# Kernel tuning notes

Measured on AMD Instinct MI355X. Metric: run time of the kernel, lower is better.

Reference implementation:

```python
import jax, jax.numpy as jnp
import numpy as np

B, S, D = 2, 1024, 2048      # batch, seq, hidden
E, F, TOP_K = 8, 1408, 2     # experts, moe intermediate, top-k


def setup_inputs() -> dict:
    key = jax.random.key(0)
    k1, k2, k3, k4, k5 = jax.random.split(key, 5)
    scale = 0.02
    return {
        "hidden_states": jax.random.normal(k1, (B, S, D), jnp.float32),
        "gate_w": jax.random.normal(k2, (E, D), jnp.float32) * scale,   # nn.Linear weight [E, D]
        "w_gate": jax.random.normal(k3, (E, D, F), jnp.float32) * scale,  # gate_proj per expert
        "w_up": jax.random.normal(k4, (E, D, F), jnp.float32) * scale,    # up_proj per expert
        "w_down": jax.random.normal(k5, (E, F, D), jnp.float32) * scale,  # down_proj per expert
    }


def reference(hidden_states, gate_w, w_gate, w_up, w_down):
    b, s, d = hidden_states.shape
    e = gate_w.shape[0]
    x = hidden_states.reshape(-1, d)                      # [T, D], T = b*s
    t = x.shape[0]

    # router: logits -> full softmax -> top-k -> renormalize (qwen_topk_softmax, normalize_topk=True)
    logits = x @ gate_w.T                                  # [T, E]
    probs = jax.nn.softmax(logits.astype(jnp.float32), axis=-1)
    top_w, sel = jax.lax.top_k(probs, TOP_K)               # [T, K]
    top_w = top_w / jnp.sum(top_w, axis=-1, keepdims=True)
    top_w = top_w.astype(logits.dtype)

    # per-token per-expert combine weight (0 for unselected experts) == weighted scatter-add
    w_te = jnp.zeros((t, e), logits.dtype).at[jnp.arange(t)[:, None], sel].add(top_w)  # [T, E]

    # expert MLPs: SiLU(x Wg) * (x Wu) -> Wd, weighted by w_te (0-weight experts contribute 0)
    g = jnp.einsum('td,edf->tef', x, w_gate)               # [T, E, F]
    u = jnp.einsum('td,edf->tef', x, w_up)                 # [T, E, F]
    h = jax.nn.silu(g) * u
    out = jnp.einsum('tef,efd->td', h * w_te[:, :, None], w_down)  # weight before down (linear, same math)
    return out.reshape(b, s, d)
```

## Files before the change

### kernel.cpp

```cpp
#include <hip/hip_runtime.h>

typedef unsigned short u16;
typedef unsigned int   u32;

#define T_TOK 2048
#define DIM   2048
#define FDIM  1408
#define NEXP  8
#define SLOTS 4224

typedef __bf16 bf16x8 __attribute__((ext_vector_type(8)));
typedef float  f32x4  __attribute__((ext_vector_type(4)));

union B16 { uint4 u; bf16x8 v; };

__device__ __forceinline__ u16 f2bf(float f) {
  union { float f; u32 u; } c; c.f = f;
  u32 u = c.u;
  u += 0x7FFFu + ((u >> 16) & 1u);
  return (u16)(u >> 16);
}
__device__ __forceinline__ float bf2f(u16 h) {
  union { u32 u; float f; } c; c.u = (u32)h << 16; return c.f;
}

__device__ __forceinline__ void gld_lds16(const void* g, void* l) {
  __builtin_amdgcn_global_load_lds(
      (const __attribute__((address_space(1))) unsigned int*)g,
      (__attribute__((address_space(3))) unsigned int*)l, 16, 0, 0);
}

__global__ __launch_bounds__(256) void cvt_transpose(
    const float* __restrict__ Wg, const float* __restrict__ Wu, const float* __restrict__ Wd,
    u16* __restrict__ WgT, u16* __restrict__ WuT, u16* __restrict__ WdT)
{
  const int z = blockIdx.z;
  const int tensor = z >> 3;
  const int e = z & 7;
  const int Kt = (tensor == 2) ? FDIM : DIM;
  const int Nt = (tensor == 2) ? DIM : FDIM;
  const float* src;
  u16* dst;
  if (tensor == 0)      { src = Wg + (size_t)e * DIM * FDIM; dst = WgT + (size_t)e * DIM * FDIM; }
  else if (tensor == 1) { src = Wu + (size_t)e * DIM * FDIM; dst = WuT + (size_t)e * DIM * FDIM; }
  else                  { src = Wd + (size_t)e * DIM * FDIM; dst = WdT + (size_t)e * DIM * FDIM; }
  const int k0 = blockIdx.y * 64, n0 = blockIdx.x * 64;
  if (k0 >= Kt || n0 >= Nt) return;

  __shared__ u16 tile[64][64 + 4];
  const int tid = threadIdx.x;
  #pragma unroll
  for (int p = 0; p < 4; ++p) {
    int k = p * 16 + (tid >> 4);
    int n = (tid & 15) * 4;
    float4 v = *(const float4*)(src + (size_t)(k0 + k) * Nt + n0 + n);
    uint2 o;
    o.x = (u32)f2bf(v.x) | ((u32)f2bf(v.y) << 16);
    o.y = (u32)f2bf(v.z) | ((u32)f2bf(v.w) << 16);
    *(uint2*)(&tile[k][n]) = o;
  }
  __syncthreads();
  #pragma unroll
  for (int p = 0; p < 4; ++p) {
    int n = tid >> 2;
    int k = (tid & 3) * 4 + p * 16;
    uint2 o;
    o.x = (u32)tile[k][n]     | ((u32)tile[k + 1][n] << 16);
    o.y = (u32)tile[k + 2][n] | ((u32)tile[k + 3][n] << 16);
    *(uint2*)(dst + (size_t)(n0 + n) * Kt + k0 + k) = o;
  }
}

__global__ __launch_bounds__(256) void router_kernel(
    const float* __restrict__ x, const float* __restrict__ gate_w,
    int* __restrict__ sel, float* __restrict__ wgt, int* __restrict__ counts)
{
  const int t = blockIdx.x;
  const float* xr = x + (size_t)t * DIM;
  float acc[NEXP];
  #pragma unroll
  for (int e = 0; e < NEXP; ++e) acc[e] = 0.f;
  for (int d = threadIdx.x; d < DIM; d += 256) {
    float xv = xr[d];
    #pragma unroll
    for (int e = 0; e < NEXP; ++e) acc[e] += xv * gate_w[e * DIM + d];
  }
  #pragma unroll
  for (int e = 0; e < NEXP; ++e) {
    #pragma unroll
    for (int s = 32; s > 0; s >>= 1) acc[e] += __shfl_down(acc[e], s, 64);
  }
  __shared__ float red[4][NEXP];
  const int lane = threadIdx.x & 63, wv = threadIdx.x >> 6;
  if (lane == 0) {
    #pragma unroll
    for (int e = 0; e < NEXP; ++e) red[wv][e] = acc[e];
  }
  __syncthreads();
  if (threadIdx.x == 0) {
    float l[NEXP];
    #pragma unroll
    for (int e = 0; e < NEXP; ++e) l[e] = red[0][e] + red[1][e] + red[2][e] + red[3][e];
    int i0 = 0;
    #pragma unroll
    for (int e = 1; e < NEXP; ++e) if (l[e] > l[i0]) i0 = e;
    int i1 = (i0 == 0) ? 1 : 0;
    #pragma unroll
    for (int e = 0; e < NEXP; ++e) if (e != i0 && l[e] > l[i1]) i1 = e;
    float w0 = 1.f / (1.f + __expf(l[i1] - l[i0]));
    sel[t * 2] = i0; sel[t * 2 + 1] = i1;
    wgt[t * 2] = w0; wgt[t * 2 + 1] = 1.f - w0;
    atomicAdd(&counts[i0], 1);
    atomicAdd(&counts[i1], 1);
  }
}

__global__ void scan_kernel(const int* __restrict__ counts, int* __restrict__ offs)
{
  if (threadIdx.x == 0) {
    int s = 0;
    for (int e = 0; e < NEXP; ++e) { offs[e] = s; s += counts[e]; }
    offs[NEXP] = s;
  }
}

__global__ __launch_bounds__(256) void gather_kernel(
    const float* __restrict__ x, const int* __restrict__ sel, const float* __restrict__ wgt,
    const int* __restrict__ offs, int* __restrict__ fill,
    int* __restrict__ slot_token, float* __restrict__ slot_w,
    int* __restrict__ tok_slots, u16* __restrict__ Xg)
{
  const int id = blockIdx.x;
  const int t = id >> 1;
  __shared__ int s_slot;
  if (threadIdx.x == 0) {
    int e = sel[id];
    int pos = atomicAdd(&fill[e], 1);
    int slot = offs[e] + pos;
    s_slot = slot;
    slot_token[slot] = t;
    slot_w[slot] = wgt[id];
    tok_slots[id] = slot;
  }
  __syncthreads();
  const int slot = s_slot;
  const float* src = x + (size_t)t * DIM + threadIdx.x * 8;
  float4 a = *(const float4*)(src);
  float4 b = *(const float4*)(src + 4);
  uint4 o;
  o.x = (u32)f2bf(a.x) | ((u32)f2bf(a.y) << 16);
  o.y = (u32)f2bf(a.z) | ((u32)f2bf(a.w) << 16);
  o.z = (u32)f2bf(b.x) | ((u32)f2bf(b.y) << 16);
  o.w = (u32)f2bf(b.z) | ((u32)f2bf(b.w) << 16);
  *(uint4*)(Xg + (size_t)slot * DIM + threadIdx.x * 8) = o;
}

__global__ __launch_bounds__(256, 2) void moe_gemm1(
    const u16* __restrict__ Xg,
    const u16* __restrict__ WgT, const u16* __restrict__ WuT,
    const int* __restrict__ offs, const float* __restrict__ slot_w,
    u16* __restrict__ H)
{
  const int e = blockIdx.z;
  const int off = offs[e];
  const int cnt = offs[e + 1] - off;
  const int m0 = blockIdx.y * 128;
  if (m0 >= cnt) return;
  const int n0 = blockIdx.x * 64;

  const u16* __restrict__ Bg_g = WgT + (size_t)e * (size_t)FDIM * DIM;
  const u16* __restrict__ Bu_g = WuT + (size_t)e * (size_t)FDIM * DIM;

  __shared__ __align__(16) u16 As[128 * 32];
  __shared__ __align__(16) u16 Bgs[64 * 32];
  __shared__ __align__(16) u16 Bus[64 * 32];

  const int tid = threadIdx.x;
  const int lane = tid & 63, wave = tid >> 6;
  const int wr = wave >> 1, wc = wave & 1;
  const int quad = lane >> 4, mr = lane & 15;

  const u16* agp0 = Xg + (size_t)(off + m0 + wave * 32 + (lane >> 2)) * DIM + (lane & 3) * 8;
  const u16* agp1 = agp0 + (size_t)16 * DIM;
  const u16* bgp  = Bg_g + (size_t)(n0 + wave * 16 + (lane >> 2)) * DIM + (lane & 3) * 8;
  const u16* bup  = Bu_g + (size_t)(n0 + wave * 16 + (lane >> 2)) * DIM + (lane & 3) * 8;
  u16* asl0 = As  + (wave * 32) * 32;
  u16* asl1 = As  + (wave * 32 + 16) * 32;
  u16* bgl  = Bgs + (wave * 16) * 32;
  u16* bul  = Bus + (wave * 16) * 32;

  f32x4 accg[4][2], accu[4][2];
  #pragma unroll
  for (int i = 0; i < 4; ++i)
    #pragma unroll
    for (int j = 0; j < 2; ++j) { accg[i][j] = {0.f,0.f,0.f,0.f}; accu[i][j] = {0.f,0.f,0.f,0.f}; }

  for (int k0 = 0; k0 < DIM; k0 += 32) {
    gld_lds16(agp0 + k0, asl0);
    gld_lds16(agp1 + k0, asl1);
    gld_lds16(bgp  + k0, bgl);
    gld_lds16(bup  + k0, bul);
    __syncthreads();
    bf16x8 af[4], bgf[2], buf2[2];
    #pragma unroll
    for (int mf = 0; mf < 4; ++mf) {
      B16 t_; t_.u = *(const uint4*)(&As[(wr * 64 + mf * 16 + mr) * 32 + quad * 8]);
      af[mf] = t_.v;
    }
    #pragma unroll
    for (int nf = 0; nf < 2; ++nf) {
      B16 tg; tg.u = *(const uint4*)(&Bgs[(wc * 32 + nf * 16 + mr) * 32 + quad * 8]);
      B16 tu; tu.u = *(const uint4*)(&Bus[(wc * 32 + nf * 16 + mr) * 32 + quad * 8]);
      bgf[nf] = tg.v; buf2[nf] = tu.v;
    }
    #pragma unroll
    for (int nf = 0; nf < 2; ++nf)
      #pragma unroll
      for (int mf = 0; mf < 4; ++mf) {
        accg[mf][nf] = __builtin_amdgcn_mfma_f32_16x16x32_bf16(af[mf], bgf[nf],  accg[mf][nf], 0, 0, 0);
        accu[mf][nf] = __builtin_amdgcn_mfma_f32_16x16x32_bf16(af[mf], buf2[nf], accu[mf][nf], 0, 0, 0);
      }
    __syncthreads();
  }

  #pragma unroll
  for (int mf = 0; mf < 4; ++mf) {
    #pragma unroll
    for (int r = 0; r < 4; ++r) {
      int row = wr * 64 + mf * 16 + quad * 4 + r;
      if (m0 + row < cnt) {
        int slot = off + m0 + row;
        float w = slot_w[slot];
        #pragma unroll
        for (int nf = 0; nf < 2; ++nf) {
          float g = accg[mf][nf][r];
          float u = accu[mf][nf][r];
          float s = g / (1.f + __expf(-g));
          H[(size_t)slot * FDIM + n0 + wc * 32 + nf * 16 + mr] = f2bf(w * s * u);
        }
      }
    }
  }
}

__global__ __launch_bounds__(256, 2) void moe_gemm2(
    const u16* __restrict__ H, const u16* __restrict__ WdT,
    const int* __restrict__ offs, u16* __restrict__ Ho)
{
  const int e = blockIdx.z;
  const int off = offs[e];
  const int cnt = offs[e + 1] - off;
  const int m0 = blockIdx.y * 128;
  if (m0 >= cnt) return;
  const int n0 = blockIdx.x * 64;

  const u16* __restrict__ Bd_g = WdT + (size_t)e * (size_t)DIM * FDIM;

  __shared__ __align__(16) u16 As[128 * 32];
  __shared__ __align__(16) u16 Bds[64 * 32];

  const int tid = threadIdx.x;
  const int lane = tid & 63, wave = tid >> 6;
  const int wr = wave >> 1, wc = wave & 1;
  const int quad = lane >> 4, mr = lane & 15;

  const u16* agp0 = H + (size_t)(off + m0 + wave * 32 + (lane >> 2)) * FDIM + (lane & 3) * 8;
  const u16* agp1 = agp0 + (size_t)16 * FDIM;
  const u16* bdp  = Bd_g + (size_t)(n0 + wave * 16 + (lane >> 2)) * FDIM + (lane & 3) * 8;
  u16* asl0 = As  + (wave * 32) * 32;
  u16* asl1 = As  + (wave * 32 + 16) * 32;
  u16* bdl  = Bds + (wave * 16) * 32;

  f32x4 acc[4][2];
  #pragma unroll
  for (int i = 0; i < 4; ++i)
    #pragma unroll
    for (int j = 0; j < 2; ++j) acc[i][j] = {0.f,0.f,0.f,0.f};

  for (int k0 = 0; k0 < FDIM; k0 += 32) {
    gld_lds16(agp0 + k0, asl0);
    gld_lds16(agp1 + k0, asl1);
    gld_lds16(bdp  + k0, bdl);
    __syncthreads();
    bf16x8 af[4], bdf[2];
    #pragma unroll
    for (int mf = 0; mf < 4; ++mf) {
      B16 t_; t_.u = *(const uint4*)(&As[(wr * 64 + mf * 16 + mr) * 32 + quad * 8]);
      af[mf] = t_.v;
    }
    #pragma unroll
    for (int nf = 0; nf < 2; ++nf) {
      B16 tb; tb.u = *(const uint4*)(&Bds[(wc * 32 + nf * 16 + mr) * 32 + quad * 8]);
      bdf[nf] = tb.v;
    }
    #pragma unroll
    for (int nf = 0; nf < 2; ++nf)
      #pragma unroll
      for (int mf = 0; mf < 4; ++mf)
        acc[mf][nf] = __builtin_amdgcn_mfma_f32_16x16x32_bf16(af[mf], bdf[nf], acc[mf][nf], 0, 0, 0);
    __syncthreads();
  }

  #pragma unroll
  for (int mf = 0; mf < 4; ++mf) {
    #pragma unroll
    for (int r = 0; r < 4; ++r) {
      int row = wr * 64 + mf * 16 + quad * 4 + r;
      if (m0 + row < cnt) {
        int slot = off + m0 + row;
        #pragma unroll
        for (int nf = 0; nf < 2; ++nf)
          Ho[(size_t)slot * DIM + n0 + wc * 32 + nf * 16 + mr] = f2bf(acc[mf][nf][r]);
      }
    }
  }
}

__global__ __launch_bounds__(256) void combine_kernel(
    const u16* __restrict__ Ho, const int* __restrict__ tok_slots,
    float* __restrict__ out)
{
  const int t = blockIdx.x;
  const int s0 = tok_slots[t * 2], s1 = tok_slots[t * 2 + 1];
  const int base = threadIdx.x * 8;
  uint4 a = *(const uint4*)(Ho + (size_t)s0 * DIM + base);
  uint4 b = *(const uint4*)(Ho + (size_t)s1 * DIM + base);
  float* o = out + (size_t)t * DIM + base;
  float4 lo, hi;
  lo.x = bf2f((u16)(a.x & 0xFFFF)) + bf2f((u16)(b.x & 0xFFFF));
  lo.y = bf2f((u16)(a.x >> 16))    + bf2f((u16)(b.x >> 16));
  lo.z = bf2f((u16)(a.y & 0xFFFF)) + bf2f((u16)(b.y & 0xFFFF));
  lo.w = bf2f((u16)(a.y >> 16))    + bf2f((u16)(b.y >> 16));
  hi.x = bf2f((u16)(a.z & 0xFFFF)) + bf2f((u16)(b.z & 0xFFFF));
  hi.y = bf2f((u16)(a.z >> 16))    + bf2f((u16)(b.z >> 16));
  hi.z = bf2f((u16)(a.w & 0xFFFF)) + bf2f((u16)(b.w & 0xFFFF));
  hi.w = bf2f((u16)(a.w >> 16))    + bf2f((u16)(b.w >> 16));
  *(float4*)(o)     = lo;
  *(float4*)(o + 4) = hi;
}

extern "C" void kernel_launch(void* const* d_in, const int* in_sizes, int n_in,
                              void* d_out, int out_size, void* d_ws, size_t ws_size,
                              hipStream_t stream) {
  const float* x      = (const float*)d_in[0];
  const float* gate_w = (const float*)d_in[1];
  const float* w_gate = (const float*)d_in[2];
  const float* w_up   = (const float*)d_in[3];
  const float* w_down = (const float*)d_in[4];
  float* out = (float*)d_out;

  char* w = (char*)d_ws;
  int*   counts     = (int*)(w + 0);
  int*   fill       = (int*)(w + 64);
  int*   offs       = (int*)(w + 128);
  int*   sel        = (int*)(w + 4096);
  float* wgt        = (float*)(w + 4096 + 16384);
  int*   tok_slots  = (int*)(w + 4096 + 2 * 16384);
  int*   slot_token = (int*)(w + 4096 + 3 * 16384);
  float* slot_w     = (float*)(w + 4096 + 3 * 16384 + 17408);
  size_t o = 131072;
  u16* Xg  = (u16*)(w + o); o += (size_t)SLOTS * DIM  * 2;
  u16* H   = (u16*)(w + o); o += (size_t)SLOTS * FDIM * 2;
  u16* Ho  = (u16*)(w + o); o += (size_t)SLOTS * DIM  * 2;
  u16* WgT = (u16*)(w + o); o += (size_t)NEXP * DIM * FDIM * 2;
  u16* WuT = (u16*)(w + o); o += (size_t)NEXP * DIM * FDIM * 2;
  u16* WdT = (u16*)(w + o); o += (size_t)NEXP * DIM * FDIM * 2;

  hipMemsetAsync(d_ws, 0, 256, stream);

  dim3 gc(32, 32, 24);
  cvt_transpose<<<gc, 256, 0, stream>>>(w_gate, w_up, w_down, WgT, WuT, WdT);

  router_kernel<<<T_TOK, 256, 0, stream>>>(x, gate_w, sel, wgt, counts);
  scan_kernel<<<1, 64, 0, stream>>>(counts, offs);
  gather_kernel<<<T_TOK * 2, 256, 0, stream>>>(x, sel, wgt, offs, fill,
                                               slot_token, slot_w, tok_slots, Xg);

  dim3 g1(FDIM / 64, 32, NEXP);
  moe_gemm1<<<g1, 256, 0, stream>>>(Xg, WgT, WuT, offs, slot_w, H);

  dim3 g2(DIM / 64, 32, NEXP);
  moe_gemm2<<<g2, 256, 0, stream>>>(H, WdT, offs, Ho);

  combine_kernel<<<T_TOK, 256, 0, stream>>>(Ho, tok_slots, out);
}
```

Baseline: 572.8 us.

## Double-buffer MoE GEMM LDS tiles, XOR-swizzle layout, widen transpose stores

Both expert GEMMs now double-buffer their LDS tiles. The next k-slice is prefetched right after a single barrier, which removes the second per-iteration barrier and overlaps global-to-LDS loads with the MFMA work. LDS chunks are XOR-swizzled by row to cut bank conflicts on the fragment reads. Launch bounds ask for 4 blocks per CU, and the M-tile grid drops to the 16 tiles actually needed. The weight transpose kernel now writes 16-byte stores instead of 8-byte ones. The trade-off is doubled LDS per block, which may limit occupancy, plus a dependence on the async load completing before the barrier.

New measurement: 575.5 us. About the same (+0.5%).

```diff
diff --git a/kernel.cpp b/kernel.cpp
--- a/kernel.cpp
+++ b/kernel.cpp
@@ -47,7 +47,7 @@
   const int k0 = blockIdx.y * 64, n0 = blockIdx.x * 64;
   if (k0 >= Kt || n0 >= Nt) return;
 
-  __shared__ u16 tile[64][64 + 4];
+  __shared__ u16 tile[64][68];
   const int tid = threadIdx.x;
   #pragma unroll
   for (int p = 0; p < 4; ++p) {
@@ -61,13 +61,18 @@
   }
   __syncthreads();
   #pragma unroll
-  for (int p = 0; p < 4; ++p) {
-    int n = tid >> 2;
-    int k = (tid & 3) * 4 + p * 16;
-    uint2 o;
-    o.x = (u32)tile[k][n]     | ((u32)tile[k + 1][n] << 16);
-    o.y = (u32)tile[k + 2][n] | ((u32)tile[k + 3][n] << 16);
-    *(uint2*)(dst + (size_t)(n0 + n) * Kt + k0 + k) = o;
+  for (int p = 0; p < 2; ++p) {
+    int n  = p * 32 + (tid >> 3);
+    int kc = (tid & 7) * 8;
+    u16 r[8];
+    #pragma unroll
+    for (int j = 0; j < 8; ++j) r[j] = tile[kc + j][n];
+    uint4 o;
+    o.x = (u32)r[0] | ((u32)r[1] << 16);
+    o.y = (u32)r[2] | ((u32)r[3] << 16);
+    o.z = (u32)r[4] | ((u32)r[5] << 16);
+    o.w = (u32)r[6] | ((u32)r[7] << 16);
+    *(uint4*)(dst + (size_t)(n0 + n) * Kt + k0 + kc) = o;
   }
 }
 
@@ -155,7 +160,7 @@
   *(uint4*)(Xg + (size_t)slot * DIM + threadIdx.x * 8) = o;
 }
 
-__global__ __launch_bounds__(256, 2) void moe_gemm1(
+__global__ __launch_bounds__(256, 4) void moe_gemm1(
     const u16* __restrict__ Xg,
     const u16* __restrict__ WgT, const u16* __restrict__ WuT,
     const int* __restrict__ offs, const float* __restrict__ slot_w,
@@ -171,23 +176,24 @@
   const u16* __restrict__ Bg_g = WgT + (size_t)e * (size_t)FDIM * DIM;
   const u16* __restrict__ Bu_g = WuT + (size_t)e * (size_t)FDIM * DIM;
 
-  __shared__ __align__(16) u16 As[128 * 32];
-  __shared__ __align__(16) u16 Bgs[64 * 32];
-  __shared__ __align__(16) u16 Bus[64 * 32];
+  __shared__ __align__(16) u16 As[2][128 * 32];
+  __shared__ __align__(16) u16 Bgs[2][64 * 32];
+  __shared__ __align__(16) u16 Bus[2][64 * 32];
 
   const int tid = threadIdx.x;
   const int lane = tid & 63, wave = tid >> 6;
   const int wr = wave >> 1, wc = wave & 1;
   const int quad = lane >> 4, mr = lane & 15;
-
-  const u16* agp0 = Xg + (size_t)(off + m0 + wave * 32 + (lane >> 2)) * DIM + (lane & 3) * 8;
+  const int qs   = (((lane & 3) ^ ((lane >> 3) & 3))) * 8;
+  const int xorc = ((quad ^ ((mr >> 1) & 3))) * 8;
+
+  const u16* agp0 = Xg + (size_t)(off + m0 + wave * 32 + (lane >> 2)) * DIM + qs;
   const u16* agp1 = agp0 + (size_t)16 * DIM;
-  const u16* bgp  = Bg_g + (size_t)(n0 + wave * 16 + (lane >> 2)) * DIM + (lane & 3) * 8;
-  const u16* bup  = Bu_g + (size_t)(n0 + wave * 16 + (lane >> 2)) * DIM + (lane & 3) * 8;
-  u16* asl0 = As  + (wave * 32) * 32;
-  u16* asl1 = As  + (wave * 32 + 16) * 32;
-  u16* bgl  = Bgs + (wave * 16) * 32;
-  u16* bul  = Bus + (wave * 16) * 32;
+  const u16* bgp  = Bg_g + (size_t)(n0 + wave * 16 + (lane >> 2)) * DIM + qs;
+  const u16* bup  = Bu_g + (size_t)(n0 + wave * 16 + (lane >> 2)) * DIM + qs;
+  const int a_lds0 = (wave * 32) * 32;
+  const int a_lds1 = (wave * 32 + 16) * 32;
+  const int b_lds  = (wave * 16) * 32;
 
   f32x4 accg[4][2], accu[4][2];
   #pragma unroll
@@ -195,22 +201,30 @@
     #pragma unroll
     for (int j = 0; j < 2; ++j) { accg[i][j] = {0.f,0.f,0.f,0.f}; accu[i][j] = {0.f,0.f,0.f,0.f}; }
 
-  for (int k0 = 0; k0 < DIM; k0 += 32) {
-    gld_lds16(agp0 + k0, asl0);
-    gld_lds16(agp1 + k0, asl1);
-    gld_lds16(bgp  + k0, bgl);
-    gld_lds16(bup  + k0, bul);
+  gld_lds16(agp0, &As[0][a_lds0]);
+  gld_lds16(agp1, &As[0][a_lds1]);
+  gld_lds16(bgp,  &Bgs[0][b_lds]);
+  gld_lds16(bup,  &Bus[0][b_lds]);
+
+  int p = 0;
+  for (int k0 = 0; k0 < DIM; k0 += 32, p ^= 1) {
     __syncthreads();
+    if (k0 + 32 < DIM) {
+      gld_lds16(agp0 + k0 + 32, &As[p ^ 1][a_lds0]);
+      gld_lds16(agp1 + k0 + 32, &As[p ^ 1][a_lds1]);
+      gld_lds16(bgp  + k0 + 32, &Bgs[p ^ 1][b_lds]);
+      gld_lds16(bup  + k0 + 32, &Bus[p ^ 1][b_lds]);
+    }
     bf16x8 af[4], bgf[2], buf2[2];
     #pragma unroll
     for (int mf = 0; mf < 4; ++mf) {
-      B16 t_; t_.u = *(const uint4*)(&As[(wr * 64 + mf * 16 + mr) * 32 + quad * 8]);
+      B16 t_; t_.u = *(const uint4*)(&As[p][(wr * 64 + mf * 16 + mr) * 32 + xorc]);
       af[mf] = t_.v;
     }
     #pragma unroll
     for (int nf = 0; nf < 2; ++nf) {
-      B16 tg; tg.u = *(const uint4*)(&Bgs[(wc * 32 + nf * 16 + mr) * 32 + quad * 8]);
-      B16 tu; tu.u = *(const uint4*)(&Bus[(wc * 32 + nf * 16 + mr) * 32 + quad * 8]);
+      B16 tg; tg.u = *(const uint4*)(&Bgs[p][(wc * 32 + nf * 16 + mr) * 32 + xorc]);
+      B16 tu; tu.u = *(const uint4*)(&Bus[p][(wc * 32 + nf * 16 + mr) * 32 + xorc]);
       bgf[nf] = tg.v; buf2[nf] = tu.v;
     }
     #pragma unroll
@@ -220,7 +234,6 @@
         accg[mf][nf] = __builtin_amdgcn_mfma_f32_16x16x32_bf16(af[mf], bgf[nf],  accg[mf][nf], 0, 0, 0);
         accu[mf][nf] = __builtin_amdgcn_mfma_f32_16x16x32_bf16(af[mf], buf2[nf], accu[mf][nf], 0, 0, 0);
       }
-    __syncthreads();
   }
 
   #pragma unroll
@@ -243,7 +256,7 @@
   }
 }
 
-__global__ __launch_bounds__(256, 2) void moe_gemm2(
+__global__ __launch_bounds__(256, 4) void moe_gemm2(
     const u16* __restrict__ H, const u16* __restrict__ WdT,
     const int* __restrict__ offs, u16* __restrict__ Ho)
 {
@@ -256,20 +269,22 @@
 
   const u16* __restrict__ Bd_g = WdT + (size_t)e * (size_t)DIM * FDIM;
 
-  __shared__ __align__(16) u16 As[128 * 32];
-  __shared__ __align__(16) u16 Bds[64 * 32];
+  __shared__ __align__(16) u16 As[2][128 * 32];
+  __shared__ __align__(16) u16 Bds[2][64 * 32];
 
   const int tid = threadIdx.x;
   const int lane = tid & 63, wave = tid >> 6;
   const int wr = wave >> 1, wc = wave & 1;
   const int quad = lane >> 4, mr = lane & 15;
-
-  const u16* agp0 = H + (size_t)(off + m0 + wave * 32 + (lane >> 2)) * FDIM + (lane & 3) * 8;
+  const int qs   = (((lane & 3) ^ ((lane >> 3) & 3))) * 8;
+  const int xorc = ((quad ^ ((mr >> 1) & 3))) * 8;
+
+  const u16* agp0 = H + (size_t)(off + m0 + wave * 32 + (lane >> 2)) * FDIM + qs;
   const u16* agp1 = agp0 + (size_t)16 * FDIM;
-  const u16* bdp  = Bd_g + (size_t)(n0 + wave * 16 + (lane >> 2)) * FDIM + (lane & 3) * 8;
-  u16* asl0 = As  + (wave * 32) * 32;
-  u16* asl1 = As  + (wave * 32 + 16) * 32;
-  u16* bdl  = Bds + (wave * 16) * 32;
+  const u16* bdp  = Bd_g + (size_t)(n0 + wave * 16 + (lane >> 2)) * FDIM + qs;
+  const int a_lds0 = (wave * 32) * 32;
+  const int a_lds1 = (wave * 32 + 16) * 32;
+  const int b_lds  = (wave * 16) * 32;
 
   f32x4 acc[4][2];
   #pragma unroll
@@ -277,20 +292,27 @@
     #pragma unroll
     for (int j = 0; j < 2; ++j) acc[i][j] = {0.f,0.f,0.f,0.f};
 
-  for (int k0 = 0; k0 < FDIM; k0 += 32) {
-    gld_lds16(agp0 + k0, asl0);
-    gld_lds16(agp1 + k0, asl1);
-    gld_lds16(bdp  + k0, bdl);
+  gld_lds16(agp0, &As[0][a_lds0]);
+  gld_lds16(agp1, &As[0][a_lds1]);
+  gld_lds16(bdp,  &Bds[0][b_lds]);
+
+  int p = 0;
+  for (int k0 = 0; k0 < FDIM; k0 += 32, p ^= 1) {
     __syncthreads();
+    if (k0 + 32 < FDIM) {
+      gld_lds16(agp0 + k0 + 32, &As[p ^ 1][a_lds0]);
+      gld_lds16(agp1 + k0 + 32, &As[p ^ 1][a_lds1]);
+      gld_lds16(bdp  + k0 + 32, &Bds[p ^ 1][b_lds]);
+    }
     bf16x8 af[4], bdf[2];
     #pragma unroll
     for (int mf = 0; mf < 4; ++mf) {
-      B16 t_; t_.u = *(const uint4*)(&As[(wr * 64 + mf * 16 + mr) * 32 + quad * 8]);
+      B16 t_; t_.u = *(const uint4*)(&As[p][(wr * 64 + mf * 16 + mr) * 32 + xorc]);
       af[mf] = t_.v;
     }
     #pragma unroll
     for (int nf = 0; nf < 2; ++nf) {
-      B16 tb; tb.u = *(const uint4*)(&Bds[(wc * 32 + nf * 16 + mr) * 32 + quad * 8]);
+      B16 tb; tb.u = *(const uint4*)(&Bds[p][(wc * 32 + nf * 16 + mr) * 32 + xorc]);
       bdf[nf] = tb.v;
     }
     #pragma unroll
@@ -298,7 +320,6 @@
       #pragma unroll
       for (int mf = 0; mf < 4; ++mf)
         acc[mf][nf] = __builtin_amdgcn_mfma_f32_16x16x32_bf16(af[mf], bdf[nf], acc[mf][nf], 0, 0, 0);
-    __syncthreads();
   }
 
   #pragma unroll
@@ -376,10 +397,10 @@
   gather_kernel<<<T_TOK * 2, 256, 0, stream>>>(x, sel, wgt, offs, fill,
                                                slot_token, slot_w, tok_slots, Xg);
 
-  dim3 g1(FDIM / 64, 32, NEXP);
+  dim3 g1(FDIM / 64, 16, NEXP);
   moe_gemm1<<<g1, 256, 0, stream>>>(Xg, WgT, WuT, offs, slot_w, H);
 
-  dim3 g2(DIM / 64, 32, NEXP);
+  dim3 g2(DIM / 64, 16, NEXP);
   moe_gemm2<<<g2, 256, 0, stream>>>(H, WdT, offs, Ho);
 
   combine_kernel<<<T_TOK, 256, 0, stream>>>(Ho, tok_slots, out);
```
